# Optimization experiments

Hardware: AMD Instinct MI355X
Metric: run time of the kernel (lower is better)

Reference implementation:

```python
import jax, jax.numpy as jnp
import numpy as np

BITS = 4
N_PACK = 32 // BITS  # int32 compression
GROUPSIZE = 128
MASK = (1 << BITS) - 1


def _unpack_int32(q, axis):
    """Unpack int32 tensor into N_PACK low-bit values along `axis`.
    Element j*N_PACK+e comes from bits [BITS*e, BITS*(e+1)) of packed word j."""
    parts = [ (q >> (BITS * e)) & MASK for e in range(N_PACK) ]
    u = jnp.stack(parts, axis=axis + 1)  # (..., P, N_PACK, ...)
    shape = list(q.shape)
    shape[axis] = shape[axis] * N_PACK
    return u.reshape(shape)


def setup_inputs() -> dict:
    key = jax.random.key(0)
    k1, k2, k3, k4, k5 = jax.random.split(key, 5)
    in_f, out_f = 4096, 12288
    tokens = 8192
    n_groups = in_f // GROUPSIZE  # 32
    x = jax.random.normal(k1, (tokens, in_f), dtype=jnp.float32)
    scales = jax.random.uniform(k2, (n_groups, out_f), dtype=jnp.float32) * 0.01 + 1e-3
    bias = jax.random.normal(k3, (out_f,), dtype=jnp.float32)
    qweight = jax.random.randint(k4, (in_f // N_PACK, out_f), jnp.iinfo(jnp.int32).min, jnp.iinfo(jnp.int32).max, dtype=jnp.int32)
    qzeros = jax.random.randint(k5, (n_groups, out_f // N_PACK), jnp.iinfo(jnp.int32).min, jnp.iinfo(jnp.int32).max, dtype=jnp.int32)
    return {"x": x, "scales": scales, "bias": bias, "qweight": qweight, "qzeros": qzeros}


def reference(x, scales, bias, qweight, qzeros):
    in_f = qweight.shape[0] * N_PACK
    out_f = qweight.shape[1]
    n_groups = scales.shape[0]
    # Unpack 4-bit weights along input-channel axis: (in_f, out_f), values 0..15
    w_int = _unpack_int32(qweight, axis=0).astype(scales.dtype)
    # Unpack zero points along output-channel axis; optimum format stores zp-1
    zp = (_unpack_int32(qzeros, axis=1) + 1).astype(scales.dtype)  # (n_groups, out_f)
    # Per-group dequant: group g covers input channels [g*GROUPSIZE, (g+1)*GROUPSIZE)
    w = (w_int.reshape(n_groups, GROUPSIZE, out_f) - zp[:, None, :]) * scales[:, None, :]
    w = w.reshape(in_f, out_f)
    # Linear: y = x @ W^T with W = w.T, i.e. x @ w
    return x @ w + bias
```

## Files before the change

### kernel.cpp

```cpp
#include <hip/hip_runtime.h>
#include <hip/hip_bf16.h>


typedef __attribute__((ext_vector_type(8))) short short8;
typedef __attribute__((ext_vector_type(4))) float f32x4;
typedef __attribute__((ext_vector_type(16))) float f32x16;

__device__ __forceinline__ short f2bf(float f) {
  unsigned u = __float_as_uint(f);
  u += 0x7fffu + ((u >> 16) & 1u);
  return (short)(u >> 16);
}

__device__ __forceinline__ void gload_lds16(const void* g, void* l) {
  __builtin_amdgcn_global_load_lds(
      (const __attribute__((address_space(1))) void*)g,
      (__attribute__((address_space(3))) void*)l,
      16, 0, 0);
}

__device__ __forceinline__ void bar() {
  asm volatile("" ::: "memory");
  __builtin_amdgcn_s_barrier();
  asm volatile("" ::: "memory");
}
__device__ __forceinline__ void wait_vm8() {
  asm volatile("s_waitcnt vmcnt(8)" ::: "memory");
}
__device__ __forceinline__ void wait_vm4() {
  asm volatile("s_waitcnt vmcnt(4)" ::: "memory");
}
__device__ __forceinline__ void wait_vm0() {
  asm volatile("s_waitcnt vmcnt(0)" ::: "memory");
}

__global__ __launch_bounds__(256) void dequant_tile_kernel(
    const int* __restrict__ qweight, const int* __restrict__ qzeros,
    const float* __restrict__ scales, short* __restrict__ Bt,
    int N, int K) {
  const int kt = K >> 5;
  const int bx = blockIdx.x;
  const int nb = bx / kt, h = bx - nb * kt;
  const int t = threadIdx.x;
  const int n = nb * 256 + t;
  const int g = h >> 2;
  const float sc = scales[(size_t)g * N + n];
  const int zw = qzeros[(size_t)g * (N >> 3) + (n >> 3)];
  const float zs = -(float)(((zw >> ((n & 7) * 4)) & 15) + 1) * sc;
  char* dst = (char*)Bt + (size_t)bx * 16384;
#pragma unroll
  for (int kw = 0; kw < 4; ++kw) {
    const int w = qweight[(size_t)(h * 4 + kw) * N + n];
    short8 v;
#pragma unroll
    for (int e = 0; e < 8; ++e)
      v[e] = f2bf(fmaf((float)((w >> (4 * e)) & 15), sc, zs));
    const int c = ((t >> 5) << 7) + ((kw >> 1) << 6) + ((kw & 1) << 5) + (t & 31);
    *(short8*)(dst + c * 16) = v;
  }
}

__global__ __launch_bounds__(256) void cvt_tile_kernel(
    const float* __restrict__ x, short* __restrict__ xb, int K) {
  const int kt = K >> 5;
  const int bx = blockIdx.x;
  const int mb = bx / kt, h = bx - mb * kt;
  const float* xs = x + (size_t)mb * 256 * K + h * 32;
  char* dst = (char*)xb + (size_t)bx * 16384;
#pragma unroll
  for (int p = 0; p < 4; ++p) {
    const int t2 = p * 256 + threadIdx.x;
    const int row = t2 >> 2, kq = t2 & 3;
    const float* s = xs + (size_t)row * K + kq * 8;
    float4 f0 = *(const float4*)s;
    float4 f1 = *(const float4*)(s + 4);
    short8 v;
    v[0] = f2bf(f0.x); v[1] = f2bf(f0.y); v[2] = f2bf(f0.z); v[3] = f2bf(f0.w);
    v[4] = f2bf(f1.x); v[5] = f2bf(f1.y); v[6] = f2bf(f1.z); v[7] = f2bf(f1.w);
    const int c = ((row >> 5) << 7) + ((kq >> 1) << 6) + ((kq & 1) << 5) + (row & 31);
    *(short8*)(dst + c * 16) = v;
  }
}

#define GBM 256
#define GBN 256

__global__ __launch_bounds__(512, 2) void gemm256_kernel(
    const short* __restrict__ At, const short* __restrict__ Bt,
    const float* __restrict__ bias, float* __restrict__ C,
    int M, int N, int K) {
  __shared__ __align__(16) char lds[4][32768];
  const int tid = threadIdx.x;
  const int nbx = N / GBN;
  const int nwg = gridDim.x;
  int bid = blockIdx.x;
  if ((nwg & 7) == 0) bid = (bid & 7) * (nwg >> 3) + (bid >> 3);
  const int mb = bid / nbx;
  const int nb = bid % nbx;
  const int bm = mb * GBM, bn = nb * GBN;

  const int wid = tid >> 6, lane = tid & 63;
  const int wr = wid >> 2, wc = wid & 3;
  const int l31 = lane & 31;
  const int lq2 = lane >> 5;

  const int P = K >> 5;

  char* lb = &lds[0][0];

  const char* aB[2];
  const char* bB[2];
  aB[0] = lb + wr * 8192 + lane * 16;
  aB[1] = aB[0] + 65536;
  bB[0] = lb + 16384 + wc * 4096 + lane * 16;
  bB[1] = bB[0] + 65536;

  const char* gA = (const char*)At + (size_t)mb * P * 16384;
  const char* gB = (const char*)Bt + (size_t)nb * P * 16384;
  char* dstA0 = lb + tid * 16;
  char* dstA1 = dstA0 + 8192;
  char* dstB0 = dstA0 + 16384;
  char* dstB1 = dstA0 + 24576;
  const size_t t16 = (size_t)tid * 16;

#define STAGE(NSL, ASRC, BSRC)                          \
  do {                                                  \
    gload_lds16((ASRC) + t16, dstA0 + (NSL) * 32768);   \
    gload_lds16((ASRC) + t16 + 8192, dstA1 + (NSL) * 32768); \
    gload_lds16((BSRC) + t16, dstB0 + (NSL) * 32768);   \
    gload_lds16((BSRC) + t16 + 8192, dstB1 + (NSL) * 32768); \
  } while (0)

  f32x16 acc[4][2] = {};

#define PHASE(SL, ST)                                                         \
  do {                                                                        \
    short8 a0[4], a1[4], b0[2], b1[2];                                        \
    _Pragma("unroll") for (int i = 0; i < 4; ++i) a0[i] =                     \
        *(const short8*)(aB[(SL) >> 1] + ((SL)&1) * 32768 + i * 2048);        \
    _Pragma("unroll") for (int j = 0; j < 2; ++j) b0[j] =                     \
        *(const short8*)(bB[(SL) >> 1] + ((SL)&1) * 32768 + j * 2048);        \
    _Pragma("unroll") for (int i = 0; i < 4; ++i) a1[i] =                     \
        *(const short8*)(aB[(SL) >> 1] + ((SL)&1) * 32768 + i * 2048 + 1024); \
    _Pragma("unroll") for (int j = 0; j < 2; ++j) b1[j] =                     \
        *(const short8*)(bB[(SL) >> 1] + ((SL)&1) * 32768 + j * 2048 + 1024); \
    if (ST) STAGE(((SL) + 3) & 3, pA + (SL)*16384, pB + (SL)*16384);          \
    __builtin_amdgcn_s_setprio(1);                                            \
    _Pragma("unroll") for (int i = 0; i < 4; ++i)                             \
        _Pragma("unroll") for (int j = 0; j < 2; ++j) acc[i][j] =             \
            __builtin_amdgcn_mfma_f32_32x32x16_bf16(a0[i], b0[j], acc[i][j],  \
                                                    0, 0, 0);                 \
    _Pragma("unroll") for (int i = 0; i < 4; ++i)                             \
        _Pragma("unroll") for (int j = 0; j < 2; ++j) acc[i][j] =             \
            __builtin_amdgcn_mfma_f32_32x32x16_bf16(a1[i], b1[j], acc[i][j],  \
                                                    0, 0, 0);                 \
    __builtin_amdgcn_s_setprio(0);                                            \
  } while (0)

  STAGE(0, gA, gB);
  STAGE(1, gA + 16384, gB + 16384);
  STAGE(2, gA + 32768, gB + 32768);

  const char* pA = gA + 3 * 16384;
  const char* pB = gB + 3 * 16384;
  const int nIt = P / 4 - 1;
  for (int it = 0; it < nIt; ++it) {
    wait_vm8(); bar(); PHASE(0, true);
    wait_vm8(); bar(); PHASE(1, true);
    wait_vm8(); bar(); PHASE(2, true);
    wait_vm8(); bar(); PHASE(3, true);
    pA += 65536; pB += 65536;
  }
  wait_vm8(); bar(); PHASE(0, true);
  wait_vm8(); bar(); PHASE(1, false);
  wait_vm4(); bar(); PHASE(2, false);
  wait_vm0(); bar(); PHASE(3, false);

#undef PHASE
#undef STAGE

  const int crow0 = bm + wr * 128 + 4 * lq2;
#pragma unroll
  for (int j = 0; j < 2; ++j) {
    const int ccol = bn + wc * 64 + j * 32 + l31;
    const float bv = bias[ccol];
#pragma unroll
    for (int i = 0; i < 4; ++i) {
#pragma unroll
      for (int reg = 0; reg < 16; ++reg) {
        const int row = crow0 + i * 32 + (reg & 3) + 8 * (reg >> 2);
        C[(size_t)row * N + ccol] = acc[i][j][reg] + bv;
      }
    }
  }
}

__global__ __launch_bounds__(256) void dequant_kernel(
    const int* __restrict__ qweight, const int* __restrict__ qzeros,
    const float* __restrict__ scales, short* __restrict__ Wt,
    int in_f, int out_f) {
  __shared__ __align__(16) short T[64][72];
  const int n0 = blockIdx.x * 64;
  const int k0 = blockIdx.y * 64;
  const int t = threadIdx.x;
  const int nl = t & 63;
  const int kw = t >> 6;
  const int n = n0 + nl;
  const int g = k0 >> 7;
  const float sc = scales[(size_t)g * out_f + n];
  const int zpw = qzeros[(size_t)g * (out_f >> 3) + (n >> 3)];
  const float zp = (float)(((zpw >> ((n & 7) * 4)) & 15) + 1);
  const float zs = zp * sc;
#pragma unroll
  for (int rr = 0; rr < 2; ++rr) {
    const int kwi = kw + rr * 4;
    const int w = qweight[(size_t)((k0 >> 3) + kwi) * out_f + n];
    short8 v;
#pragma unroll
    for (int e = 0; e < 8; ++e) {
      float f = (float)((w >> (4 * e)) & 15) * sc - zs;
      v[e] = f2bf(f);
    }
    *(short8*)&T[nl][kwi * 8] = v;
  }
  __syncthreads();
#pragma unroll
  for (int rr = 0; rr < 2; ++rr) {
    const int c = rr * 256 + t;
    const int row = c >> 3, ch = c & 7;
    *(short8*)&Wt[(size_t)(n0 + row) * in_f + k0 + ch * 8] =
        *(const short8*)&T[row][ch * 8];
  }
}

__global__ __launch_bounds__(256) void cvt_kernel(
    const float* __restrict__ x, short* __restrict__ xb, long n8) {
  long i = (long)blockIdx.x * blockDim.x + threadIdx.x;
  if (i >= n8) return;
  const float* src = x + i * 8;
  float4 a = *(const float4*)src;
  float4 b = *(const float4*)(src + 4);
  short8 v;
  v[0] = f2bf(a.x); v[1] = f2bf(a.y); v[2] = f2bf(a.z); v[3] = f2bf(a.w);
  v[4] = f2bf(b.x); v[5] = f2bf(b.y); v[6] = f2bf(b.z); v[7] = f2bf(b.w);
  *(short8*)(xb + i * 8) = v;
}

#define BM 128
#define BN 128
#define BK 64

template <bool A_BF16>
__global__ __launch_bounds__(256) void gemm_bias_kernel(
    const void* __restrict__ Av, const short* __restrict__ Bt,
    const float* __restrict__ bias, float* __restrict__ C,
    int M, int N, int K) {
  __shared__ __align__(16) short As[BM * BK];
  __shared__ __align__(16) short Bs[BN * BK];
  const int tid = threadIdx.x;
  const int bm = blockIdx.y * BM;
  const int bn = blockIdx.x * BN;
  const int wid = tid >> 6, lane = tid & 63;
  const int wr = wid >> 1, wc = wid & 1;
  const int lrow = lane & 15;
  const int lk = (lane >> 4) * 8;

  f32x4 acc[4][4] = {};

  for (int kt = 0; kt < K; kt += BK) {
    if constexpr (A_BF16) {
      const short* A = (const short*)Av;
#pragma unroll
      for (int r = 0; r < 4; ++r) {
        const int c = r * 256 + tid;
        const int row = c >> 3, ch = c & 7;
        gload_lds16(A + (size_t)(bm + row) * K + kt + ch * 8,
                    (char*)As + c * 16);
      }
    } else {
      const float* A = (const float*)Av;
#pragma unroll
      for (int r = 0; r < 4; ++r) {
        const int c = r * 256 + tid;
        const int row = c >> 3, ch = c & 7;
        const float* src = A + (size_t)(bm + row) * K + kt + ch * 8;
        float4 f0 = *(const float4*)src;
        float4 f1 = *(const float4*)(src + 4);
        short8 v;
        v[0] = f2bf(f0.x); v[1] = f2bf(f0.y); v[2] = f2bf(f0.z); v[3] = f2bf(f0.w);
        v[4] = f2bf(f1.x); v[5] = f2bf(f1.y); v[6] = f2bf(f1.z); v[7] = f2bf(f1.w);
        *(short8*)((char*)As + c * 16) = v;
      }
    }
#pragma unroll
    for (int r = 0; r < 4; ++r) {
      const int c = r * 256 + tid;
      const int row = c >> 3, ch = c & 7;
      gload_lds16(Bt + (size_t)(bn + row) * K + kt + ch * 8,
                  (char*)Bs + c * 16);
    }
    __syncthreads();
#pragma unroll
    for (int kk = 0; kk < 2; ++kk) {
      short8 af[4], bf[4];
#pragma unroll
      for (int i = 0; i < 4; ++i)
        af[i] = *(const short8*)&As[(wr * 64 + i * 16 + lrow) * BK + kk * 32 + lk];
#pragma unroll
      for (int j = 0; j < 4; ++j)
        bf[j] = *(const short8*)&Bs[(wc * 64 + j * 16 + lrow) * BK + kk * 32 + lk];
#pragma unroll
      for (int i = 0; i < 4; ++i)
#pragma unroll
        for (int j = 0; j < 4; ++j)
          acc[i][j] = __builtin_amdgcn_mfma_f32_16x16x32_bf16(
              af[i], bf[j], acc[i][j], 0, 0, 0);
    }
    __syncthreads();
  }

  const int crow0 = bm + wr * 64 + (lane >> 4) * 4;
  const int ccol0 = bn + wc * 64 + (lane & 15);
#pragma unroll
  for (int j = 0; j < 4; ++j) {
    const float bv = bias[ccol0 + j * 16];
#pragma unroll
    for (int i = 0; i < 4; ++i) {
#pragma unroll
      for (int r = 0; r < 4; ++r) {
        C[(size_t)(crow0 + i * 16 + r) * N + ccol0 + j * 16] = acc[i][j][r] + bv;
      }
    }
  }
}

__global__ __launch_bounds__(256) void naive_kernel(
    const float* __restrict__ x, const float* __restrict__ scales,
    const float* __restrict__ bias, const int* __restrict__ qw,
    const int* __restrict__ qz, float* __restrict__ out,
    int M, int K, int N) {
  long idx = (long)blockIdx.x * blockDim.x + threadIdx.x;
  if (idx >= (long)M * N) return;
  const int n = (int)(idx % N);
  const int m = (int)(idx / N);
  float acc = 0.f;
  for (int g = 0; g < K / 128; ++g) {
    const float sc = scales[(size_t)g * N + n];
    const float zp =
        (float)(((qz[(size_t)g * (N >> 3) + (n >> 3)] >> ((n & 7) * 4)) & 15) + 1);
    const float zs = zp * sc;
    for (int kw = 0; kw < 16; ++kw) {
      const int w = qw[(size_t)(g * 16 + kw) * N + n];
      const float* xp = &x[(size_t)m * K + g * 128 + kw * 8];
#pragma unroll
      for (int e = 0; e < 8; ++e)
        acc += xp[e] * ((float)((w >> (4 * e)) & 15) * sc - zs);
    }
  }
  out[idx] = acc + bias[n];
}

extern "C" void kernel_launch(void* const* d_in, const int* in_sizes, int n_in,
                              void* d_out, int out_size, void* d_ws,
                              size_t ws_size, hipStream_t stream) {
  const float* x = (const float*)d_in[0];
  const float* scales = (const float*)d_in[1];
  const float* bias = (const float*)d_in[2];
  const int* qweight = (const int*)d_in[3];
  const int* qzeros = (const int*)d_in[4];
  float* out = (float*)d_out;

  const int out_f = in_sizes[2];
  const int kwords = in_sizes[3] / out_f;
  const int in_f = kwords * 8;
  const int tokens = in_sizes[0] / in_f;
  const int M = tokens, K = in_f, N = out_f;

  const size_t wt_bytes = (size_t)K * N * sizeof(short);
  const size_t xb_bytes = (size_t)M * K * sizeof(short);

  const bool div128 = (M % BM == 0) && (N % BN == 0) && (K % BK == 0) &&
                      (K % 128 == 0) && (N % 64 == 0);
  const bool div256 = (M % GBM == 0) && (N % GBN == 0) && (K % 256 == 0);

  if (div256 && ws_size >= wt_bytes + xb_bytes) {
    short* Bt = (short*)d_ws;
    short* At = (short*)((char*)d_ws + wt_bytes);
    const int kt = K >> 5;
    dequant_tile_kernel<<<(N / 256) * kt, 256, 0, stream>>>(
        qweight, qzeros, scales, Bt, N, K);
    cvt_tile_kernel<<<(M / 256) * kt, 256, 0, stream>>>(x, At, K);
    gemm256_kernel<<<(M / GBM) * (N / GBN), 512, 0, stream>>>(
        At, Bt, bias, out, M, N, K);
  } else if (div128 && ws_size >= wt_bytes + xb_bytes) {
    short* Wt = (short*)d_ws;
    short* xb = (short*)((char*)d_ws + wt_bytes);
    dequant_kernel<<<dim3(N / 64, K / 64), 256, 0, stream>>>(
        qweight, qzeros, scales, Wt, K, N);
    const long n8 = (long)M * K / 8;
    cvt_kernel<<<(int)((n8 + 255) / 256), 256, 0, stream>>>(x, xb, n8);
    gemm_bias_kernel<true><<<dim3(N / BN, M / BM), 256, 0, stream>>>(
        xb, Wt, bias, out, M, N, K);
  } else if (div128 && ws_size >= wt_bytes) {
    short* Wt = (short*)d_ws;
    dequant_kernel<<<dim3(N / 64, K / 64), 256, 0, stream>>>(
        qweight, qzeros, scales, Wt, K, N);
    gemm_bias_kernel<false><<<dim3(N / BN, M / BM), 256, 0, stream>>>(
        x, Wt, bias, out, M, N, K);
  } else {
    const long total = (long)M * N;
    naive_kernel<<<(int)((total + 255) / 256), 256, 0, stream>>>(
        x, scales, bias, qweight, qzeros, out, M, K, N);
  }
}
```

Baseline: 815.8 us.

## Load B operand directly into registers, halving GEMM LDS footprint

The GEMM main loop no longer stages the B tile through LDS. Each wave loads its own B fragments from global memory straight into registers with inline global_load_dwordx4, prefetched two phases ahead in a 4-deep register ring, and A stays on the async global-to-LDS path. This halves shared memory per block (128KB to 64KB) and removes B LDS reads, at the cost of many more VGPRs (16 short8 buffers) and redundant B global loads across the two wave rows, which could lower occupancy or add spills. The vmcnt waits are changed to match the new per-phase load counts.

```diff
diff --git a/kernel.cpp b/kernel.cpp
--- a/kernel.cpp
+++ b/kernel.cpp
@@ -23,15 +23,6 @@
   asm volatile("" ::: "memory");
   __builtin_amdgcn_s_barrier();
   asm volatile("" ::: "memory");
-}
-__device__ __forceinline__ void wait_vm8() {
-  asm volatile("s_waitcnt vmcnt(8)" ::: "memory");
-}
-__device__ __forceinline__ void wait_vm4() {
-  asm volatile("s_waitcnt vmcnt(4)" ::: "memory");
-}
-__device__ __forceinline__ void wait_vm0() {
-  asm volatile("s_waitcnt vmcnt(0)" ::: "memory");
 }
 
 __global__ __launch_bounds__(256) void dequant_tile_kernel(
@@ -89,7 +80,7 @@
     const short* __restrict__ At, const short* __restrict__ Bt,
     const float* __restrict__ bias, float* __restrict__ C,
     int M, int N, int K) {
-  __shared__ __align__(16) char lds[4][32768];
+  __shared__ __align__(16) char lds[4][16384];
   const int tid = threadIdx.x;
   const int nbx = N / GBN;
   const int nwg = gridDim.x;
@@ -108,76 +99,92 @@
 
   char* lb = &lds[0][0];
 
-  const char* aB[2];
-  const char* bB[2];
-  aB[0] = lb + wr * 8192 + lane * 16;
-  aB[1] = aB[0] + 65536;
-  bB[0] = lb + 16384 + wc * 4096 + lane * 16;
-  bB[1] = bB[0] + 65536;
-
-  const char* gA = (const char*)At + (size_t)mb * P * 16384;
-  const char* gB = (const char*)Bt + (size_t)nb * P * 16384;
+  const char* aBase = lb + wr * 8192 + lane * 16;
+
+  const char* pAs = (const char*)At + (size_t)mb * P * 16384 + (size_t)tid * 16;
   char* dstA0 = lb + tid * 16;
   char* dstA1 = dstA0 + 8192;
-  char* dstB0 = dstA0 + 16384;
-  char* dstB1 = dstA0 + 24576;
-  const size_t t16 = (size_t)tid * 16;
-
-#define STAGE(NSL, ASRC, BSRC)                          \
-  do {                                                  \
-    gload_lds16((ASRC) + t16, dstA0 + (NSL) * 32768);   \
-    gload_lds16((ASRC) + t16 + 8192, dstA1 + (NSL) * 32768); \
-    gload_lds16((BSRC) + t16, dstB0 + (NSL) * 32768);   \
-    gload_lds16((BSRC) + t16 + 8192, dstB1 + (NSL) * 32768); \
+
+  const char* pBb = (const char*)Bt + (size_t)nb * P * 16384 + wc * 4096 +
+                    (size_t)lane * 16;
+
+  short8 bs[4][4];
+
+#define STAGEA(NSL, SRC)                                    \
+  do {                                                      \
+    gload_lds16((SRC), dstA0 + (NSL) * 16384);              \
+    gload_lds16((SRC) + 8192, dstA1 + (NSL) * 16384);       \
   } while (0)
 
+#define LOADB(SET, SRC)                                              \
+  do {                                                               \
+    asm volatile("global_load_dwordx4 %0, %1, off"                   \
+                 : "=v"(bs[SET][0]) : "v"((SRC)));                   \
+    asm volatile("global_load_dwordx4 %0, %1, off"                   \
+                 : "=v"(bs[SET][1]) : "v"((SRC) + 1024));            \
+    asm volatile("global_load_dwordx4 %0, %1, off"                   \
+                 : "=v"(bs[SET][2]) : "v"((SRC) + 2048));            \
+    asm volatile("global_load_dwordx4 %0, %1, off"                   \
+                 : "=v"(bs[SET][3]) : "v"((SRC) + 3072));            \
+  } while (0)
+
+#define WAITB(NSTR, SET)                                                  \
+  asm volatile("s_waitcnt vmcnt(" NSTR ")"                                \
+               : "+v"(bs[SET][0]), "+v"(bs[SET][1]), "+v"(bs[SET][2]),    \
+                 "+v"(bs[SET][3])::"memory")
+
   f32x16 acc[4][2] = {};
 
-#define PHASE(SL, ST)                                                         \
+#define PHASE(SL, STG, LDB, WN)                                               \
   do {                                                                        \
-    short8 a0[4], a1[4], b0[2], b1[2];                                        \
-    _Pragma("unroll") for (int i = 0; i < 4; ++i) a0[i] =                     \
-        *(const short8*)(aB[(SL) >> 1] + ((SL)&1) * 32768 + i * 2048);        \
-    _Pragma("unroll") for (int j = 0; j < 2; ++j) b0[j] =                     \
-        *(const short8*)(bB[(SL) >> 1] + ((SL)&1) * 32768 + j * 2048);        \
-    _Pragma("unroll") for (int i = 0; i < 4; ++i) a1[i] =                     \
-        *(const short8*)(aB[(SL) >> 1] + ((SL)&1) * 32768 + i * 2048 + 1024); \
-    _Pragma("unroll") for (int j = 0; j < 2; ++j) b1[j] =                     \
-        *(const short8*)(bB[(SL) >> 1] + ((SL)&1) * 32768 + j * 2048 + 1024); \
-    if (ST) STAGE(((SL) + 3) & 3, pA + (SL)*16384, pB + (SL)*16384);          \
+    WAITB(WN, SL);                                                            \
+    bar();                                                                    \
+    short8 a[4][2];                                                           \
+    _Pragma("unroll") for (int i = 0; i < 4; ++i)                             \
+        _Pragma("unroll") for (int kh = 0; kh < 2; ++kh) a[i][kh] =           \
+        *(const short8*)(aBase + (SL)*16384 + i * 2048 + kh * 1024);          \
+    if (STG) STAGEA(((SL) + 3) & 3, pAo + (SL) * 16384);                      \
+    if (LDB) LOADB(((SL) + 2) & 3, pBo + (SL) * 16384);                       \
     __builtin_amdgcn_s_setprio(1);                                            \
-    _Pragma("unroll") for (int i = 0; i < 4; ++i)                             \
+    _Pragma("unroll") for (int kh = 0; kh < 2; ++kh)                          \
+        _Pragma("unroll") for (int i = 0; i < 4; ++i)                         \
         _Pragma("unroll") for (int j = 0; j < 2; ++j) acc[i][j] =             \
-            __builtin_amdgcn_mfma_f32_32x32x16_bf16(a0[i], b0[j], acc[i][j],  \
-                                                    0, 0, 0);                 \
-    _Pragma("unroll") for (int i = 0; i < 4; ++i)                             \
-        _Pragma("unroll") for (int j = 0; j < 2; ++j) acc[i][j] =             \
-            __builtin_amdgcn_mfma_f32_32x32x16_bf16(a1[i], b1[j], acc[i][j],  \
-                                                    0, 0, 0);                 \
+            __builtin_amdgcn_mfma_f32_32x32x16_bf16(                          \
+                a[i][kh], bs[SL][j * 2 + kh], acc[i][j], 0, 0, 0);            \
     __builtin_amdgcn_s_setprio(0);                                            \
   } while (0)
 
-  STAGE(0, gA, gB);
-  STAGE(1, gA + 16384, gB + 16384);
-  STAGE(2, gA + 32768, gB + 32768);
-
-  const char* pA = gA + 3 * 16384;
-  const char* pB = gB + 3 * 16384;
+  STAGEA(0, pAs);
+  LOADB(0, pBb);
+  STAGEA(1, pAs + 16384);
+  LOADB(1, pBb + 16384);
+  STAGEA(2, pAs + 32768);
+
+  size_t pAoff = 3 * 16384, pBoff = 2 * 16384;
   const int nIt = P / 4 - 1;
   for (int it = 0; it < nIt; ++it) {
-    wait_vm8(); bar(); PHASE(0, true);
-    wait_vm8(); bar(); PHASE(1, true);
-    wait_vm8(); bar(); PHASE(2, true);
-    wait_vm8(); bar(); PHASE(3, true);
-    pA += 65536; pB += 65536;
-  }
-  wait_vm8(); bar(); PHASE(0, true);
-  wait_vm8(); bar(); PHASE(1, false);
-  wait_vm4(); bar(); PHASE(2, false);
-  wait_vm0(); bar(); PHASE(3, false);
+    const char* pAo = pAs + pAoff;
+    const char* pBo = pBb + pBoff;
+    PHASE(0, true, true, "6");
+    PHASE(1, true, true, "6");
+    PHASE(2, true, true, "6");
+    PHASE(3, true, true, "6");
+    pAoff += 65536;
+    pBoff += 65536;
+  }
+  {
+    const char* pAo = pAs + pAoff;
+    const char* pBo = pBb + pBoff;
+    PHASE(0, true, true, "6");
+    PHASE(1, false, true, "6");
+    PHASE(2, false, false, "4");
+    PHASE(3, false, false, "0");
+  }
 
 #undef PHASE
-#undef STAGE
+#undef WAITB
+#undef LOADB
+#undef STAGEA
 
   const int crow0 = bm + wr * 128 + 4 * lq2;
 #pragma unroll
@@ -384,14 +391,14 @@
   const bool div256 = (M % GBM == 0) && (N % GBN == 0) && (K % 256 == 0);
 
   if (div256 && ws_size >= wt_bytes + xb_bytes) {
-    short* Bt = (short*)d_ws;
-    short* At = (short*)((char*)d_ws + wt_bytes);
+    short* Btile = (short*)d_ws;
+    short* Atile = (short*)((char*)d_ws + wt_bytes);
     const int kt = K >> 5;
     dequant_tile_kernel<<<(N / 256) * kt, 256, 0, stream>>>(
-        qweight, qzeros, scales, Bt, N, K);
-    cvt_tile_kernel<<<(M / 256) * kt, 256, 0, stream>>>(x, At, K);
+        qweight, qzeros, scales, Btile, N, K);
+    cvt_tile_kernel<<<(M / 256) * kt, 256, 0, stream>>>(x, Atile, K);
     gemm256_kernel<<<(M / GBM) * (N / GBN), 512, 0, stream>>>(
-        At, Bt, bias, out, M, N, K);
+        Atile, Btile, bias, out, M, N, K);
   } else if (div128 && ws_size >= wt_bytes + xb_bytes) {
     short* Wt = (short*)d_ws;
     short* xb = (short*)((char*)d_ws + wt_bytes);
```

New measurement: 843.4 us. 1.03x slower.
